# Performance work log

Measured on AMD Instinct MI355X. Metric: run time of the kernel, lower is better.

## Reference

```python
import jax, jax.numpy as jnp
import numpy as np

N = 8192
F_X = 48       # raw node feature dim
F_RW = 16      # random-walk feature dim
IN_DIM = F_X + F_RW   # 64
H1 = 128
H2 = 64
N_BRANCH = 4   # hop0 (identity) + hop1..hop3


def setup_inputs() -> dict:
    key = jax.random.key(0)
    ks = jax.random.split(key, 9)
    x = jax.random.normal(ks[0], (N, F_X), dtype=jnp.float32)
    walk_feats = jax.random.normal(ks[1], (N, F_RW), dtype=jnp.float32)
    hop1 = jax.random.uniform(ks[2], (N, N), dtype=jnp.float32)
    hop2 = jax.random.uniform(ks[3], (N, N), dtype=jnp.float32)
    hop3 = jax.random.uniform(ks[4], (N, N), dtype=jnp.float32)
    # Stacked params for the 4 parallel 2-layer MLPs (layer0..layer3)
    s1 = 1.0 / np.sqrt(IN_DIM)
    s2 = 1.0 / np.sqrt(H1)
    W1 = jax.random.uniform(ks[5], (N_BRANCH, IN_DIM, H1), dtype=jnp.float32, minval=-s1, maxval=s1)
    b1 = jax.random.uniform(ks[6], (N_BRANCH, H1), dtype=jnp.float32, minval=-s1, maxval=s1)
    W2 = jax.random.uniform(ks[7], (N_BRANCH, H1, H2), dtype=jnp.float32, minval=-s2, maxval=s2)
    b2 = jax.random.uniform(ks[8], (N_BRANCH, H2), dtype=jnp.float32, minval=-s2, maxval=s2)
    return {"x": x, "walk_feats": walk_feats, "hop1": hop1, "hop2": hop2,
            "hop3": hop3, "W1": W1, "b1": b1, "W2": W2, "b2": b2}


def reference(x, walk_feats, hop1, hop2, hop3, W1, b1, W2, b2):
    # X = cat(x, walk_feats) along feature dim (use_rw=True)
    X = jnp.concatenate([x, walk_feats], axis=1)          # [N, IN_DIM]
    # Branch inputs: hop0 uses X directly; hops 1-3 aggregate via adjacency matmul
    hops = jnp.stack([X, hop1 @ X, hop2 @ X, hop3 @ X])   # [4, N, IN_DIM]
    # Parallel 2-layer MLPs: Linear -> ReLU -> Linear, per branch k
    h = jax.nn.relu(jnp.einsum('knf,kfh->knh', hops, W1) + b1[:, None, :])  # [4, N, H1]
    out = jnp.einsum('knh,kho->kno', h, W2) + b2[:, None, :]                 # [4, N, H2]
    return out.sum(axis=0)                                                   # [N, H2]
```

## Files before the change

### kernel.cpp

```cpp
#include <hip/hip_runtime.h>
#include <stdint.h>


#define N_NODES 8192
#define NDIM 64

typedef __attribute__((ext_vector_type(8))) short short8;
typedef __attribute__((ext_vector_type(4))) float f32x4;

__device__ __forceinline__ unsigned int f2bf(float f) {
  unsigned int u = __builtin_bit_cast(unsigned int, f);
  u += 0x7fffu + ((u >> 16) & 1u);
  return u >> 16;
}

__global__ void prep_kernel(const float* __restrict__ x,
                            const float* __restrict__ wf,
                            unsigned short* __restrict__ Bp) {
  int s = blockIdx.x * 256 + threadIdx.x;
  int khi = s >> 9;
  int rem = s & 511;
  int n   = rem >> 3;
  int klo = rem & 7;
  int k   = (khi << 3) | klo;
  float v = (n < 48) ? x[k * 48 + n] : wf[k * 16 + (n - 48)];
  Bp[s] = (unsigned short)f2bf(v);
}

__global__ __launch_bounds__(256, 6) void hop_gemm(
    const float* __restrict__ hop1,
    const float* __restrict__ hop2,
    const float* __restrict__ hop3,
    const unsigned short* __restrict__ Bp,
    float* __restrict__ Y) {
  __shared__ __attribute__((aligned(16))) float red[4 * 1024];

  int bid  = blockIdx.x;
  int h    = bid % 3;
  int mblk = bid / 3;
  const float* A = (h == 0) ? hop1 : (h == 1) ? hop2 : hop3;

  int tid  = threadIdx.x;
  int w    = tid >> 6;
  int lane = tid & 63;
  int n0   = lane & 15;
  int q    = lane >> 4;

  int rowA = mblk * 16 + n0;
  const float* Arow = A + (size_t)rowA * N_NODES + w * 2048 + q * 8;
  const short8* Bw  = (const short8*)Bp + ((size_t)(w * 256 + q)) * 64 + n0;

  f32x4 acc0 = {0.f, 0.f, 0.f, 0.f};
  f32x4 acc1 = {0.f, 0.f, 0.f, 0.f};
  f32x4 acc2 = {0.f, 0.f, 0.f, 0.f};
  f32x4 acc3 = {0.f, 0.f, 0.f, 0.f};

  float4 xa0, xa1, ya0, ya1;
  short8 xb0, xb1, xb2, xb3;
  short8 yb0, yb1, yb2, yb3;

#define LOAD_A(s, A0, A1)                                \
  do {                                                   \
    const float* _p = Arow + 32 * (s);                   \
    A0 = *(const float4*)_p;                             \
    A1 = *(const float4*)(_p + 4);                       \
  } while (0)

#define LOAD_B(s, B0, B1, B2, B3)                        \
  do {                                                   \
    const short8* _p = Bw + 256 * (s);                   \
    B0 = _p[0]; B1 = _p[16]; B2 = _p[32]; B3 = _p[48];   \
  } while (0)

#define PROC(A0, A1, B0, B1, B2, B3)                                        \
  do {                                                                      \
    union { short8 s; unsigned int u[4]; } af;                              \
    af.u[0] = (f2bf((A0).y) << 16) | f2bf((A0).x);                          \
    af.u[1] = (f2bf((A0).w) << 16) | f2bf((A0).z);                          \
    af.u[2] = (f2bf((A1).y) << 16) | f2bf((A1).x);                          \
    af.u[3] = (f2bf((A1).w) << 16) | f2bf((A1).z);                          \
    acc0 = __builtin_amdgcn_mfma_f32_16x16x32_bf16(af.s, B0, acc0, 0, 0, 0);\
    acc1 = __builtin_amdgcn_mfma_f32_16x16x32_bf16(af.s, B1, acc1, 0, 0, 0);\
    acc2 = __builtin_amdgcn_mfma_f32_16x16x32_bf16(af.s, B2, acc2, 0, 0, 0);\
    acc3 = __builtin_amdgcn_mfma_f32_16x16x32_bf16(af.s, B3, acc3, 0, 0, 0);\
  } while (0)

  LOAD_A(0, xa0, xa1);
  LOAD_B(0, xb0, xb1, xb2, xb3);
#pragma unroll 1
  for (int s = 0; s < 62; s += 2) {
    LOAD_A(s + 1, ya0, ya1);
    LOAD_B(s + 1, yb0, yb1, yb2, yb3);
    PROC(xa0, xa1, xb0, xb1, xb2, xb3);
    LOAD_A(s + 2, xa0, xa1);
    LOAD_B(s + 2, xb0, xb1, xb2, xb3);
    PROC(ya0, ya1, yb0, yb1, yb2, yb3);
  }
  LOAD_A(63, ya0, ya1);
  LOAD_B(63, yb0, yb1, yb2, yb3);
  PROC(xa0, xa1, xb0, xb1, xb2, xb3);
  PROC(ya0, ya1, yb0, yb1, yb2, yb3);

#undef LOAD_A
#undef LOAD_B
#undef PROC

  {
    float* rw = &red[w * 1024 + lane * 4];
    *(f32x4*)(rw)       = acc0;
    *(f32x4*)(rw + 256) = acc1;
    *(f32x4*)(rw + 512) = acc2;
    *(f32x4*)(rw + 768) = acc3;
  }
  __syncthreads();

  {
    int t = tid;
    f32x4 v = *(const f32x4*)&red[t * 4];
    v += *(const f32x4*)&red[1024 + t * 4];
    v += *(const f32x4*)&red[2048 + t * 4];
    v += *(const f32x4*)&red[3072 + t * 4];

    int nt    = t >> 6;
    int lane2 = t & 63;
    int q2    = lane2 >> 4;
    int n02   = lane2 & 15;
    int col   = nt * 16 + n02;
    float* Yo = Y + (size_t)h * (N_NODES * NDIM)
                  + (size_t)(mblk * 16 + q2 * 4) * NDIM + col;
    Yo[0 * NDIM] = v.x;
    Yo[1 * NDIM] = v.y;
    Yo[2 * NDIM] = v.z;
    Yo[3 * NDIM] = v.w;
  }
}

#define YS_LD 68
#define HS_LD 132
__global__ __launch_bounds__(256) void mlp_kernel(
    const float* __restrict__ x, const float* __restrict__ wf,
    const float* __restrict__ Y,
    const float* __restrict__ W1, const float* __restrict__ b1,
    const float* __restrict__ W2, const float* __restrict__ b2,
    float* __restrict__ out) {
  __shared__ __attribute__((aligned(16))) float Ys[16 * YS_LD];
  __shared__ __attribute__((aligned(16))) float Hs[16 * HS_LD];
  __shared__ float b1s[128];
  __shared__ float b2s[64];

  int t = threadIdx.x;
  int rowBase = blockIdx.x * 16;

  int r  = t >> 4;
  int c8 = (t & 15) * 8;
  int c4 = (t & 15) * 4;

  float oacc[4] = {0.f, 0.f, 0.f, 0.f};

  for (int k = 0; k < 4; ++k) {
    for (int i = t; i < 16 * 64; i += 256) {
      int row = i >> 6;
      int n   = i & 63;
      float v;
      if (k == 0) {
        int grow = rowBase + row;
        v = (n < 48) ? x[grow * 48 + n] : wf[grow * 16 + (n - 48)];
      } else {
        v = Y[(size_t)(k - 1) * (N_NODES * 64) + (size_t)(rowBase + row) * 64 + n];
      }
      Ys[row * YS_LD + n] = v;
    }
    if (t < 128) b1s[t] = b1[k * 128 + t];
    else if (t < 192) b2s[t - 128] = b2[k * 64 + (t - 128)];
    __syncthreads();

    const float* W1k = W1 + k * 8192;
    float f0 = 0.f, f1 = 0.f, f2 = 0.f, f3 = 0.f;
    float f4 = 0.f, f5 = 0.f, f6 = 0.f, f7 = 0.f;
#pragma unroll 4
    for (int kk = 0; kk < 64; ++kk) {
      float yv = Ys[r * YS_LD + kk];
      float4 w0 = *(const float4*)&W1k[kk * 128 + c8];
      float4 w1 = *(const float4*)&W1k[kk * 128 + c8 + 4];
      f0 = fmaf(yv, w0.x, f0); f1 = fmaf(yv, w0.y, f1);
      f2 = fmaf(yv, w0.z, f2); f3 = fmaf(yv, w0.w, f3);
      f4 = fmaf(yv, w1.x, f4); f5 = fmaf(yv, w1.y, f5);
      f6 = fmaf(yv, w1.z, f6); f7 = fmaf(yv, w1.w, f7);
    }
    {
      float4 ba = *(const float4*)&b1s[c8];
      float4 bb = *(const float4*)&b1s[c8 + 4];
      float4 h0, h1;
      h0.x = fmaxf(f0 + ba.x, 0.f); h0.y = fmaxf(f1 + ba.y, 0.f);
      h0.z = fmaxf(f2 + ba.z, 0.f); h0.w = fmaxf(f3 + ba.w, 0.f);
      h1.x = fmaxf(f4 + bb.x, 0.f); h1.y = fmaxf(f5 + bb.y, 0.f);
      h1.z = fmaxf(f6 + bb.z, 0.f); h1.w = fmaxf(f7 + bb.w, 0.f);
      *(float4*)&Hs[r * HS_LD + c8]     = h0;
      *(float4*)&Hs[r * HS_LD + c8 + 4] = h1;
    }
    __syncthreads();

    const float* W2k = W2 + k * 8192;
    float o0 = b2s[c4], o1 = b2s[c4 + 1], o2 = b2s[c4 + 2], o3 = b2s[c4 + 3];
#pragma unroll 4
    for (int kk = 0; kk < 128; ++kk) {
      float hv = Hs[r * HS_LD + kk];
      float4 wv = *(const float4*)&W2k[kk * 64 + c4];
      o0 = fmaf(hv, wv.x, o0); o1 = fmaf(hv, wv.y, o1);
      o2 = fmaf(hv, wv.z, o2); o3 = fmaf(hv, wv.w, o3);
    }
    oacc[0] += o0; oacc[1] += o1; oacc[2] += o2; oacc[3] += o3;
    __syncthreads();
  }

  float4 v;
  v.x = oacc[0]; v.y = oacc[1]; v.z = oacc[2]; v.w = oacc[3];
  *(float4*)&out[(size_t)(rowBase + r) * 64 + c4] = v;
}

extern "C" void kernel_launch(void* const* d_in, const int* in_sizes, int n_in,
                              void* d_out, int out_size, void* d_ws, size_t ws_size,
                              hipStream_t stream) {
  const float* x    = (const float*)d_in[0];
  const float* wf   = (const float*)d_in[1];
  const float* hop1 = (const float*)d_in[2];
  const float* hop2 = (const float*)d_in[3];
  const float* hop3 = (const float*)d_in[4];
  const float* W1   = (const float*)d_in[5];
  const float* b1   = (const float*)d_in[6];
  const float* W2   = (const float*)d_in[7];
  const float* b2   = (const float*)d_in[8];
  float* out = (float*)d_out;

  unsigned short* Bp = (unsigned short*)d_ws;
  float* Y = (float*)((char*)d_ws + (1 << 20));

  prep_kernel<<<dim3(524288 / 256), dim3(256), 0, stream>>>(x, wf, Bp);
  hop_gemm<<<dim3(1536), dim3(256), 0, stream>>>(hop1, hop2, hop3, Bp, Y);
  mlp_kernel<<<dim3(512), dim3(256), 0, stream>>>(x, wf, Y, W1, b1, W2, b2, out);
}
```

Measured before the change: 827.3 us.

## Stage hop matrix tiles into LDS via async global_load_lds double buffering

The A-operand (hop adjacency rows) is now streamed into a double-buffered, XOR-swizzled LDS tile using direct global-to-LDS 16-byte copies, instead of each lane loading scattered 32-byte pieces from 16 rows straight into registers. Each wave instruction now fetches a contiguous 1KB row segment, which should improve coalescing and keep more memory traffic in flight while MFMAs consume the previous tile. In exchange it adds a block barrier per 256-wide K tile and 32KB of LDS per block, with the occupancy hint lowered from 6 to 5. The reduction buffer reuses the staging LDS.

```diff
diff --git a/kernel.cpp b/kernel.cpp
--- a/kernel.cpp
+++ b/kernel.cpp
@@ -4,6 +4,8 @@
 
 #define N_NODES 8192
 #define NDIM 64
+#define K_TILE 256
+#define NT (N_NODES / K_TILE)
 
 typedef __attribute__((ext_vector_type(8))) short short8;
 typedef __attribute__((ext_vector_type(4))) float f32x4;
@@ -12,6 +14,12 @@
   unsigned int u = __builtin_bit_cast(unsigned int, f);
   u += 0x7fffu + ((u >> 16) & 1u);
   return u >> 16;
+}
+
+__device__ __forceinline__ void async_copy16(void* lds, const void* g) {
+  __builtin_amdgcn_global_load_lds(
+      (const __attribute__((address_space(1))) void*)g,
+      (__attribute__((address_space(3))) void*)lds, 16, 0, 0);
 }
 
 __global__ void prep_kernel(const float* __restrict__ x,
@@ -27,13 +35,13 @@
   Bp[s] = (unsigned short)f2bf(v);
 }
 
-__global__ __launch_bounds__(256, 6) void hop_gemm(
+__global__ __launch_bounds__(256, 5) void hop_gemm(
     const float* __restrict__ hop1,
     const float* __restrict__ hop2,
     const float* __restrict__ hop3,
     const unsigned short* __restrict__ Bp,
     float* __restrict__ Y) {
-  __shared__ __attribute__((aligned(16))) float red[4 * 1024];
+  __shared__ __attribute__((aligned(16))) float bufA[2][16 * K_TILE];
 
   int bid  = blockIdx.x;
   int h    = bid % 3;
@@ -45,68 +53,79 @@
   int lane = tid & 63;
   int n0   = lane & 15;
   int q    = lane >> 4;
-
-  int rowA = mblk * 16 + n0;
-  const float* Arow = A + (size_t)rowA * N_NODES + w * 2048 + q * 8;
-  const short8* Bw  = (const short8*)Bp + ((size_t)(w * 256 + q)) * 64 + n0;
+  int lane16 = lane << 4;
+
+  const short8* Bp8 = (const short8*)Bp;
+
+  const char* gA[4];
+  int ldsOff[4];
+#pragma unroll
+  for (int i = 0; i < 4; ++i) {
+    int row = w * 4 + i;
+    gA[i] = (const char*)A + ((size_t)(mblk * 16 + row) << 15)
+            + (unsigned)(lane16 ^ ((row & 7) << 4));
+    ldsOff[i] = row << 10;
+  }
 
   f32x4 acc0 = {0.f, 0.f, 0.f, 0.f};
   f32x4 acc1 = {0.f, 0.f, 0.f, 0.f};
   f32x4 acc2 = {0.f, 0.f, 0.f, 0.f};
   f32x4 acc3 = {0.f, 0.f, 0.f, 0.f};
 
-  float4 xa0, xa1, ya0, ya1;
-  short8 xb0, xb1, xb2, xb3;
-  short8 yb0, yb1, yb2, yb3;
-
-#define LOAD_A(s, A0, A1)                                \
-  do {                                                   \
-    const float* _p = Arow + 32 * (s);                   \
-    A0 = *(const float4*)_p;                             \
-    A1 = *(const float4*)(_p + 4);                       \
+  int swz = (n0 & 7) << 4;
+
+#define STAGE(tt)                                                  \
+  do {                                                             \
+    char* db = (char*)bufA[(tt) & 1];                              \
+    _Pragma("unroll")                                              \
+    for (int i = 0; i < 4; ++i) {                                  \
+      async_copy16(db + ldsOff[i], gA[i] + ((size_t)(tt) << 10));  \
+    }                                                              \
   } while (0)
 
-#define LOAD_B(s, B0, B1, B2, B3)                        \
-  do {                                                   \
-    const short8* _p = Bw + 256 * (s);                   \
-    B0 = _p[0]; B1 = _p[16]; B2 = _p[32]; B3 = _p[48];   \
+#define KSTEP(lbuf, khb, s)                                                  \
+  do {                                                                       \
+    int off0 = (n0 << 10) + ((((w << 8) + ((s) << 7)) + (q << 5)) ^ swz);    \
+    float4 a0 = *(const float4*)((const char*)(lbuf) + off0);                \
+    float4 a1 = *(const float4*)((const char*)(lbuf) + (off0 ^ 16));         \
+    const short8* bp = Bp8 + (size_t)(((khb) + (s) * 4 + q) * 64 + n0);      \
+    short8 b0 = bp[0], b1 = bp[16], b2 = bp[32], b3 = bp[48];                \
+    union { short8 v; unsigned int u[4]; } af;                               \
+    af.u[0] = (f2bf(a0.y) << 16) | f2bf(a0.x);                               \
+    af.u[1] = (f2bf(a0.w) << 16) | f2bf(a0.z);                               \
+    af.u[2] = (f2bf(a1.y) << 16) | f2bf(a1.x);                               \
+    af.u[3] = (f2bf(a1.w) << 16) | f2bf(a1.z);                               \
+    acc0 = __builtin_amdgcn_mfma_f32_16x16x32_bf16(af.v, b0, acc0, 0, 0, 0); \
+    acc1 = __builtin_amdgcn_mfma_f32_16x16x32_bf16(af.v, b1, acc1, 0, 0, 0); \
+    acc2 = __builtin_amdgcn_mfma_f32_16x16x32_bf16(af.v, b2, acc2, 0, 0, 0); \
+    acc3 = __builtin_amdgcn_mfma_f32_16x16x32_bf16(af.v, b3, acc3, 0, 0, 0); \
   } while (0)
 
-#define PROC(A0, A1, B0, B1, B2, B3)                                        \
-  do {                                                                      \
-    union { short8 s; unsigned int u[4]; } af;                              \
-    af.u[0] = (f2bf((A0).y) << 16) | f2bf((A0).x);                          \
-    af.u[1] = (f2bf((A0).w) << 16) | f2bf((A0).z);                          \
-    af.u[2] = (f2bf((A1).y) << 16) | f2bf((A1).x);                          \
-    af.u[3] = (f2bf((A1).w) << 16) | f2bf((A1).z);                          \
-    acc0 = __builtin_amdgcn_mfma_f32_16x16x32_bf16(af.s, B0, acc0, 0, 0, 0);\
-    acc1 = __builtin_amdgcn_mfma_f32_16x16x32_bf16(af.s, B1, acc1, 0, 0, 0);\
-    acc2 = __builtin_amdgcn_mfma_f32_16x16x32_bf16(af.s, B2, acc2, 0, 0, 0);\
-    acc3 = __builtin_amdgcn_mfma_f32_16x16x32_bf16(af.s, B3, acc3, 0, 0, 0);\
-  } while (0)
-
-  LOAD_A(0, xa0, xa1);
-  LOAD_B(0, xb0, xb1, xb2, xb3);
+  STAGE(0);
+  __syncthreads();
+
 #pragma unroll 1
-  for (int s = 0; s < 62; s += 2) {
-    LOAD_A(s + 1, ya0, ya1);
-    LOAD_B(s + 1, yb0, yb1, yb2, yb3);
-    PROC(xa0, xa1, xb0, xb1, xb2, xb3);
-    LOAD_A(s + 2, xa0, xa1);
-    LOAD_B(s + 2, xb0, xb1, xb2, xb3);
-    PROC(ya0, ya1, yb0, yb1, yb2, yb3);
-  }
-  LOAD_A(63, ya0, ya1);
-  LOAD_B(63, yb0, yb1, yb2, yb3);
-  PROC(xa0, xa1, xb0, xb1, xb2, xb3);
-  PROC(ya0, ya1, yb0, yb1, yb2, yb3);
-
-#undef LOAD_A
-#undef LOAD_B
-#undef PROC
-
+  for (int t = 0; t < NT - 1; ++t) {
+    STAGE(t + 1);
+    const float* lbuf = bufA[t & 1];
+    int khb = t * 32 + w * 8;
+    KSTEP(lbuf, khb, 0);
+    KSTEP(lbuf, khb, 1);
+    __syncthreads();
+  }
   {
-    float* rw = &red[w * 1024 + lane * 4];
+    const float* lbuf = bufA[(NT - 1) & 1];
+    int khb = (NT - 1) * 32 + w * 8;
+    KSTEP(lbuf, khb, 0);
+    KSTEP(lbuf, khb, 1);
+  }
+
+#undef STAGE
+#undef KSTEP
+
+  float* red = (float*)bufA;
+  {
+    float* rw = red + w * 1024 + lane * 4;
     *(f32x4*)(rw)       = acc0;
     *(f32x4*)(rw + 256) = acc1;
     *(f32x4*)(rw + 512) = acc2;
```

After: 762.1 us. 1.09x faster.

## Stage hop GEMM tiles through LDS with multi-buffered async global_load_lds

Applied to the files above, without the earlier changes.

The hop GEMM now streams A (fp32 hop rows) and B tiles into a 5-deep LDS ring using async global_load_lds copies, with vmcnt waits and barriers. It also changes the work split: each wave owns 16 output columns over the full K instead of a quarter of K over all columns, which removes the cross-wave LDS reduction. The A tile is XOR-swizzled to avoid LDS bank conflicts. The intent is deeper memory-level parallelism to keep the bandwidth-bound 3x8192x8192 fp32 reads streaming. In exchange it uses much more LDS, lowers the launch-bounds occupancy hint to 2, and adds per-tile barriers.

```diff
diff --git a/kernel.cpp b/kernel.cpp
--- a/kernel.cpp
+++ b/kernel.cpp
@@ -4,6 +4,12 @@
 
 #define N_NODES 8192
 #define NDIM 64
+#define K_TILE 64
+#define NT (N_NODES / K_TILE)
+#define ABYTES 4096
+#define BBYTES 8192
+#define BUFB (ABYTES + BBYTES)
+#define NBUF 5
 
 typedef __attribute__((ext_vector_type(8))) short short8;
 typedef __attribute__((ext_vector_type(4))) float f32x4;
@@ -12,6 +18,12 @@
   unsigned int u = __builtin_bit_cast(unsigned int, f);
   u += 0x7fffu + ((u >> 16) & 1u);
   return u >> 16;
+}
+
+__device__ __forceinline__ void async_copy16(void* lds, const void* g) {
+  __builtin_amdgcn_global_load_lds(
+      (const __attribute__((address_space(1))) void*)g,
+      (__attribute__((address_space(3))) void*)lds, 16, 0, 0);
 }
 
 __global__ void prep_kernel(const float* __restrict__ x,
@@ -27,13 +39,13 @@
   Bp[s] = (unsigned short)f2bf(v);
 }
 
-__global__ __launch_bounds__(256, 6) void hop_gemm(
+__global__ __launch_bounds__(256, 2) void hop_gemm(
     const float* __restrict__ hop1,
     const float* __restrict__ hop2,
     const float* __restrict__ hop3,
     const unsigned short* __restrict__ Bp,
     float* __restrict__ Y) {
-  __shared__ __attribute__((aligned(16))) float red[4 * 1024];
+  __shared__ __attribute__((aligned(16))) char ldsbuf[NBUF * BUFB];
 
   int bid  = blockIdx.x;
   int h    = bid % 3;
@@ -45,93 +57,92 @@
   int lane = tid & 63;
   int n0   = lane & 15;
   int q    = lane >> 4;
-
-  int rowA = mblk * 16 + n0;
-  const float* Arow = A + (size_t)rowA * N_NODES + w * 2048 + q * 8;
-  const short8* Bw  = (const short8*)Bp + ((size_t)(w * 256 + q)) * 64 + n0;
-
-  f32x4 acc0 = {0.f, 0.f, 0.f, 0.f};
-  f32x4 acc1 = {0.f, 0.f, 0.f, 0.f};
-  f32x4 acc2 = {0.f, 0.f, 0.f, 0.f};
-  f32x4 acc3 = {0.f, 0.f, 0.f, 0.f};
-
-  float4 xa0, xa1, ya0, ya1;
-  short8 xb0, xb1, xb2, xb3;
-  short8 yb0, yb1, yb2, yb3;
-
-#define LOAD_A(s, A0, A1)                                \
-  do {                                                   \
-    const float* _p = Arow + 32 * (s);                   \
-    A0 = *(const float4*)_p;                             \
-    A1 = *(const float4*)(_p + 4);                       \
+  int swz  = (n0 & 7) << 4;
+  int wn0  = w * 16 + n0;
+
+  int arow = w * 4 + (lane >> 4);
+  const char* gAsrc = (const char*)A
+      + ((size_t)(mblk * 16 + arow) << 15)
+      + (unsigned)((((lane & 15) << 4) ^ ((arow & 7) << 4)));
+  const char* gBsrc = (const char*)Bp + ((w * 2) << 10) + (lane << 4);
+
+  f32x4 acc = {0.f, 0.f, 0.f, 0.f};
+
+#define STAGE(tt, bo_)                                                      \
+  do {                                                                      \
+    char* db = ldsbuf + (bo_);                                              \
+    async_copy16(db + (w << 10), gAsrc + ((size_t)(tt) << 8));              \
+    async_copy16(db + ABYTES + ((w * 2) << 10),                             \
+                 gBsrc + ((size_t)(tt) << 13));                             \
+    async_copy16(db + ABYTES + ((w * 2 + 1) << 10),                         \
+                 gBsrc + ((size_t)(tt) << 13) + 1024);                      \
   } while (0)
 
-#define LOAD_B(s, B0, B1, B2, B3)                        \
-  do {                                                   \
-    const short8* _p = Bw + 256 * (s);                   \
-    B0 = _p[0]; B1 = _p[16]; B2 = _p[32]; B3 = _p[48];   \
+#define KSTEP(bo_, ks)                                                       \
+  do {                                                                      \
+    const char* pA = ldsbuf + (bo_);                                        \
+    int off0 = (n0 << 8) + ((((ks) << 7) + (q << 5)) ^ swz);                \
+    float4 a0 = *(const float4*)(pA + off0);                                \
+    float4 a1 = *(const float4*)(pA + (off0 ^ 16));                         \
+    const short8* bp = (const short8*)(pA + ABYTES)                         \
+                       + (((ks) * 4 + q) * 64 + wn0);                       \
+    short8 b0 = bp[0];                                                      \
+    union { short8 v; unsigned int u[4]; } af;                              \
+    af.u[0] = (f2bf(a0.y) << 16) | f2bf(a0.x);                              \
+    af.u[1] = (f2bf(a0.w) << 16) | f2bf(a0.z);                              \
+    af.u[2] = (f2bf(a1.y) << 16) | f2bf(a1.x);                              \
+    af.u[3] = (f2bf(a1.w) << 16) | f2bf(a1.z);                              \
+    acc = __builtin_amdgcn_mfma_f32_16x16x32_bf16(af.v, b0, acc, 0, 0, 0);  \
   } while (0)
 
-#define PROC(A0, A1, B0, B1, B2, B3)                                        \
+#define WAIT_BAR(n)                                                         \
   do {                                                                      \
-    union { short8 s; unsigned int u[4]; } af;                              \
-    af.u[0] = (f2bf((A0).y) << 16) | f2bf((A0).x);                          \
-    af.u[1] = (f2bf((A0).w) << 16) | f2bf((A0).z);                          \
-    af.u[2] = (f2bf((A1).y) << 16) | f2bf((A1).x);                          \
-    af.u[3] = (f2bf((A1).w) << 16) | f2bf((A1).z);                          \
-    acc0 = __builtin_amdgcn_mfma_f32_16x16x32_bf16(af.s, B0, acc0, 0, 0, 0);\
-    acc1 = __builtin_amdgcn_mfma_f32_16x16x32_bf16(af.s, B1, acc1, 0, 0, 0);\
-    acc2 = __builtin_amdgcn_mfma_f32_16x16x32_bf16(af.s, B2, acc2, 0, 0, 0);\
-    acc3 = __builtin_amdgcn_mfma_f32_16x16x32_bf16(af.s, B3, acc3, 0, 0, 0);\
+    asm volatile("s_waitcnt vmcnt(" #n ")" ::: "memory");                   \
+    __builtin_amdgcn_s_barrier();                                           \
+    __builtin_amdgcn_sched_barrier(0);                                      \
   } while (0)
 
-  LOAD_A(0, xa0, xa1);
-  LOAD_B(0, xb0, xb1, xb2, xb3);
+  STAGE(0, 0 * BUFB);
+  STAGE(1, 1 * BUFB);
+  STAGE(2, 2 * BUFB);
+  STAGE(3, 3 * BUFB);
+  STAGE(4, 4 * BUFB);
+
+  int bo = 0;
 #pragma unroll 1
-  for (int s = 0; s < 62; s += 2) {
-    LOAD_A(s + 1, ya0, ya1);
-    LOAD_B(s + 1, yb0, yb1, yb2, yb3);
-    PROC(xa0, xa1, xb0, xb1, xb2, xb3);
-    LOAD_A(s + 2, xa0, xa1);
-    LOAD_B(s + 2, xb0, xb1, xb2, xb3);
-    PROC(ya0, ya1, yb0, yb1, yb2, yb3);
+  for (int t = 0; t < NT - NBUF; ++t) {
+    WAIT_BAR(12);
+    KSTEP(bo, 0);
+    KSTEP(bo, 1);
+    asm volatile("s_waitcnt lgkmcnt(0)" ::: "memory");
+    __builtin_amdgcn_sched_barrier(0);
+    __builtin_amdgcn_s_barrier();
+    STAGE(t + NBUF, bo);
+    bo += BUFB;
+    if (bo == NBUF * BUFB) bo = 0;
   }
-  LOAD_A(63, ya0, ya1);
-  LOAD_B(63, yb0, yb1, yb2, yb3);
-  PROC(xa0, xa1, xb0, xb1, xb2, xb3);
-  PROC(ya0, ya1, yb0, yb1, yb2, yb3);
-
-#undef LOAD_A
-#undef LOAD_B
-#undef PROC
+
+  WAIT_BAR(12); KSTEP(bo, 0); KSTEP(bo, 1);
+  bo += BUFB; if (bo == NBUF * BUFB) bo = 0;
+  WAIT_BAR(9);  KSTEP(bo, 0); KSTEP(bo, 1);
+  bo += BUFB; if (bo == NBUF * BUFB) bo = 0;
+  WAIT_BAR(6);  KSTEP(bo, 0); KSTEP(bo, 1);
+  bo += BUFB; if (bo == NBUF * BUFB) bo = 0;
+  WAIT_BAR(3);  KSTEP(bo, 0); KSTEP(bo, 1);
+  bo += BUFB; if (bo == NBUF * BUFB) bo = 0;
+  WAIT_BAR(0);  KSTEP(bo, 0); KSTEP(bo, 1);
+
+#undef STAGE
+#undef KSTEP
+#undef WAIT_BAR
 
   {
-    float* rw = &red[w * 1024 + lane * 4];
-    *(f32x4*)(rw)       = acc0;
-    *(f32x4*)(rw + 256) = acc1;
-    *(f32x4*)(rw + 512) = acc2;
-    *(f32x4*)(rw + 768) = acc3;
-  }
-  __syncthreads();
-
-  {
-    int t = tid;
-    f32x4 v = *(const f32x4*)&red[t * 4];
-    v += *(const f32x4*)&red[1024 + t * 4];
-    v += *(const f32x4*)&red[2048 + t * 4];
-    v += *(const f32x4*)&red[3072 + t * 4];
-
-    int nt    = t >> 6;
-    int lane2 = t & 63;
-    int q2    = lane2 >> 4;
-    int n02   = lane2 & 15;
-    int col   = nt * 16 + n02;
     float* Yo = Y + (size_t)h * (N_NODES * NDIM)
-                  + (size_t)(mblk * 16 + q2 * 4) * NDIM + col;
-    Yo[0 * NDIM] = v.x;
-    Yo[1 * NDIM] = v.y;
-    Yo[2 * NDIM] = v.z;
-    Yo[3 * NDIM] = v.w;
+                  + (size_t)(mblk * 16 + q * 4) * NDIM + wn0;
+    Yo[0 * NDIM] = acc.x;
+    Yo[1 * NDIM] = acc.y;
+    Yo[2 * NDIM] = acc.z;
+    Yo[3 * NDIM] = acc.w;
   }
 }
 
```

Measured after the change: 910.1 us. +10.0%, slower.
